# Optimization experiments

Measured on AMD Instinct MI355X. Metric: run time of the kernel, lower is better.

Reference implementation:

```python
import jax, jax.numpy as jnp
import numpy as np

N_NODES = 100_000
N_EDGES = 1_000_000
LATENT = 64
HID_ATOM = 256
HID_BOND = 256
RBF_DIM = 32
RBF_DMAX = 10.0
N_ATOM_TYPES = 10
N_CHARGES = 6
N_BOND_ORDERS = 5


def setup_inputs() -> dict:
    key = jax.random.key(0)
    ks = jax.random.split(key, 12)
    positions = jax.random.normal(ks[0], (N_NODES, 3), dtype=jnp.float32) * 5.0
    quantized = jax.random.normal(ks[1], (N_NODES, LATENT), dtype=jnp.float32)
    pair_indices = jax.random.randint(ks[2], (N_EDGES, 2), 0, N_NODES, dtype=jnp.int64)
    s = 0.05
    return {
        "positions": positions,
        "quantized": quantized,
        "pair_indices": pair_indices,
        "aW1": jax.random.normal(ks[3], (LATENT, HID_ATOM), jnp.float32) * s,
        "ab1": jnp.zeros((HID_ATOM,), jnp.float32),
        "aW2": jax.random.normal(ks[4], (HID_ATOM, N_ATOM_TYPES + N_CHARGES), jnp.float32) * s,
        "ab2": jnp.zeros((N_ATOM_TYPES + N_CHARGES,), jnp.float32),
        "bW1": jax.random.normal(ks[5], (LATENT + RBF_DIM, HID_BOND), jnp.float32) * s,
        "bb1": jnp.zeros((HID_BOND,), jnp.float32),
        "bW2": jax.random.normal(ks[6], (HID_BOND, N_BOND_ORDERS), jnp.float32) * s,
        "bb2": jnp.zeros((N_BOND_ORDERS,), jnp.float32),
    }


def _norm_no_nan(x, eps=1e-8):
    # L2 norm over last axis, clamped to avoid NaN gradients at 0
    return jnp.sqrt(jnp.maximum(jnp.sum(x * x, axis=-1), eps))


def _rbf(D, D_min=0.0, D_max=RBF_DMAX, D_count=RBF_DIM):
    mu = jnp.linspace(D_min, D_max, D_count, dtype=D.dtype)  # [D_count]
    sigma = (D_max - D_min) / D_count
    z = (D[..., None] - mu) / sigma
    return jnp.exp(-z * z)  # [E, D_count]


def reference(positions, quantized, pair_indices, aW1, ab1, aW2, ab2, bW1, bb1, bW2, bb2):
    src = pair_indices[:, 0]
    dst = pair_indices[:, 1]
    # pairwise distances -> RBF expansion
    x_i = positions[src]            # [E, 3]
    x_j = positions[dst]
    dists = _rbf(_norm_no_nan(x_i - x_j))  # [E, rbf_dim]
    # atom decoder (per node)
    h = jax.nn.relu(quantized @ aW1 + ab1)
    scalar_logits = h @ aW2 + ab2
    atom_type_logits = scalar_logits[:, :N_ATOM_TYPES]
    atom_charge_logits = scalar_logits[:, N_ATOM_TYPES:]
    # bond decoder (per edge): gathered latent sum concat RBF
    pair_feats = quantized[src] + quantized[dst]           # [E, latent]
    combined = jnp.concatenate([pair_feats, dists], axis=1)  # [E, latent+rbf]
    hb = jax.nn.relu(combined @ bW1 + bb1)
    bond_order_logits = hb @ bW2 + bb2
    return (atom_type_logits, atom_charge_logits, bond_order_logits)
```

## Files before the change

kernel.cpp:

```cpp
#include <hip/hip_runtime.h>
#include <hip/hip_bf16.h>

typedef __bf16 bf16x8 __attribute__((ext_vector_type(8)));
typedef __bf16 bf16x4 __attribute__((ext_vector_type(4)));
typedef float  f32x4  __attribute__((ext_vector_type(4)));
typedef short  s16x4  __attribute__((ext_vector_type(4)));

#define N_NODES 100000
#define N_EDGES 1000000
#define LATENT  64
#define HID     256
#define RBF_DIM 32
#define NTYPES  10
#define NCHG    6
#define NBOND   5

#define ATOM_TILES (N_NODES / 32)
#define ANBLK 512

#define ETILE  32
#define ETILES (N_EDGES / ETILE)
#define ENBLK  1280

static __device__ __forceinline__ f32x4 mfma16(bf16x4 a, bf16x4 b, f32x4 c) {
#if __has_builtin(__builtin_amdgcn_mfma_f32_16x16x16bf16_1k)
    s16x4 ai = __builtin_bit_cast(s16x4, a);
    s16x4 bi = __builtin_bit_cast(s16x4, b);
    return __builtin_amdgcn_mfma_f32_16x16x16bf16_1k(ai, bi, c, 0, 0, 0);
#else
    asm volatile("s_nop 1\n\t"
                 "v_mfma_f32_16x16x16_bf16 %0, %1, %2, %0\n\t"
                 "s_nop 7\n\ts_nop 7"
                 : "+v"(c) : "v"(a), "v"(b));
    return c;
#endif
}

struct __align__(16) ASmem {
    __bf16 qs[32][72];
    __bf16 hsE[32][264];
    float  red[4][2][4][64];
};

template<bool EMIT_QB>
__global__ __launch_bounds__(256, 2) void atom_kernel(
    const float* __restrict__ q,   const float* __restrict__ aW1,
    const float* __restrict__ ab1, const float* __restrict__ aW2,
    const float* __restrict__ ab2, float* __restrict__ outA,
    float* __restrict__ outB,      __bf16* __restrict__ qb,
    const float* __restrict__ pos, const int* __restrict__ pair,
    float* __restrict__ dist)
{
    __shared__ ASmem sm;
    const int t    = threadIdx.x;
    const int w    = t >> 6;
    const int lane = t & 63;
    const int l15  = lane & 15;
    const int hi   = lane >> 4;
    const int wcol = w * 64;

    bf16x8 aw1f[2][4];
    #pragma unroll
    for (int kb = 0; kb < 2; ++kb)
        #pragma unroll
        for (int nt = 0; nt < 4; ++nt) {
            const int nn = wcol + nt * 16 + l15;
            const int k0 = kb * 32 + hi * 8;
            bf16x8 v;
            #pragma unroll
            for (int j = 0; j < 8; ++j) v[j] = (__bf16)aW1[(k0 + j) * HID + nn];
            aw1f[kb][nt] = v;
        }
    bf16x8 aw2f[2];
    #pragma unroll
    for (int kk = 0; kk < 2; ++kk) {
        const int k0 = (w * 2 + kk) * 32 + hi * 8;
        bf16x8 v;
        #pragma unroll
        for (int j = 0; j < 8; ++j) v[j] = (__bf16)aW2[(k0 + j) * 16 + l15];
        aw2f[kk] = v;
    }
    float4 b1v[4];
    #pragma unroll
    for (int nt = 0; nt < 4; ++nt)
        b1v[nt] = *(const float4*)(&ab1[wcol + nt * 16 + hi * 4]);

    const int m_st = t >> 3;
    const int p_st = t & 7;

    for (int tile = blockIdx.x; tile < ATOM_TILES; tile += ANBLK) {
        const int node0 = tile * 32;
        {
            const float* qr = q + (size_t)(node0 + m_st) * 64 + p_st * 8;
            const float4 a0 = *(const float4*)(qr);
            const float4 a1 = *(const float4*)(qr + 4);
            bf16x8 v;
            v[0] = (__bf16)a0.x; v[1] = (__bf16)a0.y; v[2] = (__bf16)a0.z; v[3] = (__bf16)a0.w;
            v[4] = (__bf16)a1.x; v[5] = (__bf16)a1.y; v[6] = (__bf16)a1.z; v[7] = (__bf16)a1.w;
            *(bf16x8*)(&sm.qs[m_st][p_st * 8]) = v;
            if constexpr (EMIT_QB)
                *(bf16x8*)(qb + (size_t)(node0 + m_st) * 64 + p_st * 8) = v;
        }
        __syncthreads();

        f32x4 acc[2][4];
        #pragma unroll
        for (int mt = 0; mt < 2; ++mt)
            #pragma unroll
            for (int nt = 0; nt < 4; ++nt)
                #pragma unroll
                for (int r = 0; r < 4; ++r)
                    acc[mt][nt][r] = ((const float*)&b1v[nt])[r];

        #pragma unroll
        for (int kb = 0; kb < 2; ++kb)
            #pragma unroll
            for (int mt = 0; mt < 2; ++mt) {
                const bf16x8 bq = *(const bf16x8*)((const char*)&sm.qs[0][0]
                                   + (mt * 16 + l15) * 144 + kb * 64 + hi * 16);
                #pragma unroll
                for (int nt = 0; nt < 4; ++nt)
                    acc[mt][nt] = __builtin_amdgcn_mfma_f32_16x16x32_bf16(
                        aw1f[kb][nt], bq, acc[mt][nt], 0, 0, 0);
            }

        #pragma unroll
        for (int mt = 0; mt < 2; ++mt)
            #pragma unroll
            for (int nt = 0; nt < 4; ++nt) {
                bf16x4 hv;
                #pragma unroll
                for (int r = 0; r < 4; ++r)
                    hv[r] = (__bf16)fmaxf(acc[mt][nt][r], 0.f);
                *(bf16x4*)(&sm.hsE[mt * 16 + l15][wcol + nt * 16 + hi * 4]) = hv;
            }
        __syncthreads();

        f32x4 acc2[2];
        {
            f32x4 z = {0.f, 0.f, 0.f, 0.f};
            acc2[0] = z; acc2[1] = z;
        }
        #pragma unroll
        for (int mt = 0; mt < 2; ++mt)
            #pragma unroll
            for (int kk = 0; kk < 2; ++kk) {
                const int kb = w * 2 + kk;
                const bf16x8 af = *(const bf16x8*)((const char*)&sm.hsE[0][0]
                                   + (mt * 16 + l15) * 528 + kb * 64 + hi * 16);
                acc2[mt] = __builtin_amdgcn_mfma_f32_16x16x32_bf16(
                    af, aw2f[kk], acc2[mt], 0, 0, 0);
            }
        #pragma unroll
        for (int mt = 0; mt < 2; ++mt)
            #pragma unroll
            for (int r = 0; r < 4; ++r)
                sm.red[w][mt][r][lane] = acc2[mt][r];
        __syncthreads();

        {
            const int o  = t & 15;
            const int m0 = t >> 4;
            #pragma unroll
            for (int half = 0; half < 2; ++half) {
                const int m  = m0 + half * 16;
                const int mt = m >> 4, rr = m & 15;
                const int hh = rr >> 2, r = rr & 3;
                float s = ab2[o];
                #pragma unroll
                for (int ww = 0; ww < 4; ++ww) s += sm.red[ww][mt][r][hh * 16 + o];
                const int node = node0 + m;
                if (o < NTYPES) outA[node * NTYPES + o] = s;
                else            outB[node * NCHG + (o - NTYPES)] = s;
            }
        }
        __syncthreads();
    }

    if constexpr (EMIT_QB) {
        for (int e = blockIdx.x * 256 + t; e < N_EDGES; e += ANBLK * 256) {
            const int2 pr = ((const int2*)pair)[e];
            const float dx = pos[(unsigned)pr.x * 3u]      - pos[(unsigned)pr.y * 3u];
            const float dy = pos[(unsigned)pr.x * 3u + 1u] - pos[(unsigned)pr.y * 3u + 1u];
            const float dz = pos[(unsigned)pr.x * 3u + 2u] - pos[(unsigned)pr.y * 3u + 2u];
            dist[e] = sqrtf(fmaxf(dx * dx + dy * dy + dz * dz, 1e-8f));
        }
    }
}

struct __align__(16) ESmem {
    __bf16 comb[2][ETILE][104];
    float  red[2][4][2][4][64];
};

__device__ __forceinline__ void bar_lgkm() {
    asm volatile("s_waitcnt lgkmcnt(0)" ::: "memory");
    __builtin_amdgcn_s_barrier();
}

template<bool USEBF>
__global__ __launch_bounds__(256, 3) void edge_kernel(
    const float* __restrict__ pos, const float* __restrict__ qf,
    const __bf16* __restrict__ qb, const float* __restrict__ dist,
    const int* __restrict__ pair,
    const float* __restrict__ bW1, const float* __restrict__ bb1,
    const float* __restrict__ bW2, const float* __restrict__ bb2,
    float* __restrict__ outC)
{
    __shared__ ESmem sm;
    const int t    = threadIdx.x;
    const int w    = t >> 6;
    const int lane = t & 63;
    const int l15  = lane & 15;
    const int hi   = lane >> 4;
    const int hid0 = w * 64;

    bf16x8 bw1f[3][4];
    #pragma unroll
    for (int kb = 0; kb < 3; ++kb)
        #pragma unroll
        for (int nt = 0; nt < 4; ++nt) {
            const int nn = hid0 + nt * 16 + l15;
            const int k0 = kb * 32 + hi * 8;
            bf16x8 v;
            #pragma unroll
            for (int j = 0; j < 8; ++j) v[j] = (__bf16)bW1[(k0 + j) * HID + nn];
            bw1f[kb][nt] = v;
        }
    bf16x4 w2f[4];
    #pragma unroll
    for (int nt = 0; nt < 4; ++nt) {
        bf16x4 v;
        #pragma unroll
        for (int j = 0; j < 4; ++j)
            v[j] = (l15 < NBOND)
                 ? (__bf16)bW2[(hid0 + nt * 16 + hi * 4 + j) * NBOND + l15]
                 : (__bf16)0.f;
        w2f[nt] = v;
    }
    float4 b1v[4];
    #pragma unroll
    for (int nt = 0; nt < 4; ++nt)
        b1v[nt] = *(const float4*)(&bb1[hid0 + nt * 16 + hi * 4]);

    const int e_loc = t >> 3;
    const int p     = t & 7;

    int tile = blockIdx.x;
    bf16x8 gs, gd;
    float  Dv;
    float4 fs0, fs1, fd0, fd1;
    float  ps0, ps1, ps2, pd0, pd1, pd2;

    #define GATHER(pN, tg)                                                        \
        if constexpr (USEBF) {                                                    \
            gs = *(const bf16x8*)(qb + ((unsigned)(pN).x * 64u + (unsigned)(p*8)));\
            gd = *(const bf16x8*)(qb + ((unsigned)(pN).y * 64u + (unsigned)(p*8)));\
            Dv = dist[(size_t)(tg) * ETILE + e_loc];                              \
        } else {                                                                  \
            fs0 = *(const float4*)(qf + ((unsigned)(pN).x * 64u + (unsigned)(p*8)));     \
            fs1 = *(const float4*)(qf + ((unsigned)(pN).x * 64u + (unsigned)(p*8) + 4u));\
            fd0 = *(const float4*)(qf + ((unsigned)(pN).y * 64u + (unsigned)(p*8)));     \
            fd1 = *(const float4*)(qf + ((unsigned)(pN).y * 64u + (unsigned)(p*8) + 4u));\
            ps0 = pos[(unsigned)(pN).x * 3u];  ps1 = pos[(unsigned)(pN).x * 3u + 1u];    \
            ps2 = pos[(unsigned)(pN).x * 3u + 2u];                                \
            pd0 = pos[(unsigned)(pN).y * 3u];  pd1 = pos[(unsigned)(pN).y * 3u + 1u];    \
            pd2 = pos[(unsigned)(pN).y * 3u + 2u];                                \
        }

    #define STAGE(buf)                                                            \
        {                                                                         \
            bf16x8 cv;                                                            \
            float D;                                                              \
            if constexpr (USEBF) {                                                \
                _Pragma("unroll")                                                 \
                for (int j = 0; j < 8; ++j)                                       \
                    cv[j] = (__bf16)((float)gs[j] + (float)gd[j]);                \
                D = Dv;                                                           \
            } else {                                                              \
                cv[0] = (__bf16)(fs0.x + fd0.x); cv[1] = (__bf16)(fs0.y + fd0.y); \
                cv[2] = (__bf16)(fs0.z + fd0.z); cv[3] = (__bf16)(fs0.w + fd0.w); \
                cv[4] = (__bf16)(fs1.x + fd1.x); cv[5] = (__bf16)(fs1.y + fd1.y); \
                cv[6] = (__bf16)(fs1.z + fd1.z); cv[7] = (__bf16)(fs1.w + fd1.w); \
                const float dx = ps0 - pd0, dy = ps1 - pd1, dz = ps2 - pd2;       \
                D = sqrtf(fmaxf(dx * dx + dy * dy + dz * dz, 1e-8f));             \
            }                                                                     \
            *(bf16x8*)(&sm.comb[buf][e_loc][p * 8]) = cv;                         \
            bf16x4 rv;                                                            \
            _Pragma("unroll")                                                     \
            for (int j = 0; j < 4; ++j) {                                         \
                const float mu = (float)(p * 4 + j) * (10.0f / 31.0f);            \
                const float z  = (D - mu) * 3.2f;                                 \
                rv[j] = (__bf16)__expf(-z * z);                                   \
            }                                                                     \
            *(bf16x4*)(&sm.comb[buf][e_loc][64 + p * 4]) = rv;                    \
        }

    int  tgA = tile;
    int2 pA  = ((const int2*)pair)[(size_t)tile * ETILE + e_loc];
    GATHER(pA, tgA);
    tgA = (tile + ENBLK < ETILES) ? tile + ENBLK : 0;
    pA  = ((const int2*)pair)[(size_t)tgA * ETILE + e_loc];
    STAGE(0);
    GATHER(pA, tgA);
    tgA = (tile + 2 * ENBLK < ETILES) ? tile + 2 * ENBLK : 0;
    pA  = ((const int2*)pair)[(size_t)tgA * ETILE + e_loc];
    bar_lgkm();

    int cur = 0;
    int e0_prev = -1;

    for (; tile < ETILES; tile += ENBLK) {
        const int e0 = tile * ETILE;

        if (e0_prev >= 0 && t < 160) {
            const int m = t / 5, o = t % 5;
            const int mt = m >> 4, rr = m & 15;
            const int hh = rr >> 2, r = rr & 3;
            float s = bb2[o];
            #pragma unroll
            for (int ww = 0; ww < 4; ++ww)
                s += sm.red[cur ^ 1][ww][mt][r][hh * 16 + o];
            outC[(size_t)(e0_prev + m) * NBOND + o] = s;
        }

        STAGE(cur ^ 1);

        GATHER(pA, tgA);
        tgA = (tile + 3 * ENBLK < ETILES) ? tile + 3 * ENBLK : 0;
        pA  = ((const int2*)pair)[(size_t)tgA * ETILE + e_loc];

        f32x4 acc[2][4];
        #pragma unroll
        for (int mt = 0; mt < 2; ++mt)
            #pragma unroll
            for (int nt = 0; nt < 4; ++nt)
                #pragma unroll
                for (int r = 0; r < 4; ++r)
                    acc[mt][nt][r] = ((const float*)&b1v[nt])[r];

        #pragma unroll
        for (int kb = 0; kb < 3; ++kb)
            #pragma unroll
            for (int mt = 0; mt < 2; ++mt) {
                const bf16x8 bf = *(const bf16x8*)((const char*)&sm.comb[cur][0][0]
                                   + (mt * 16 + l15) * 208 + kb * 64 + hi * 16);
                #pragma unroll
                for (int nt = 0; nt < 4; ++nt)
                    acc[mt][nt] = __builtin_amdgcn_mfma_f32_16x16x32_bf16(
                        bw1f[kb][nt], bf, acc[mt][nt], 0, 0, 0);
            }

        {
            f32x4 acc2[2];
            {
                f32x4 z = {0.f, 0.f, 0.f, 0.f};
                acc2[0] = z; acc2[1] = z;
            }
            #pragma unroll
            for (int mt = 0; mt < 2; ++mt)
                #pragma unroll
                for (int nt = 0; nt < 4; ++nt) {
                    bf16x4 hv;
                    #pragma unroll
                    for (int r = 0; r < 4; ++r)
                        hv[r] = (__bf16)fmaxf(acc[mt][nt][r], 0.f);
                    acc2[mt] = mfma16(hv, w2f[nt], acc2[mt]);
                }
            #pragma unroll
            for (int mt = 0; mt < 2; ++mt)
                #pragma unroll
                for (int r = 0; r < 4; ++r)
                    sm.red[cur][w][mt][r][lane] = acc2[mt][r];
        }

        e0_prev = e0;
        bar_lgkm();
        cur ^= 1;
    }

    if (e0_prev >= 0 && t < 160) {
        const int m = t / 5, o = t % 5;
        const int mt = m >> 4, rr = m & 15;
        const int hh = rr >> 2, r = rr & 3;
        float s = bb2[o];
        #pragma unroll
        for (int ww = 0; ww < 4; ++ww)
            s += sm.red[cur ^ 1][ww][mt][r][hh * 16 + o];
        outC[(size_t)(e0_prev + m) * NBOND + o] = s;
    }
    #undef GATHER
    #undef STAGE
}

extern "C" void kernel_launch(void* const* d_in, const int* in_sizes, int n_in,
                              void* d_out, int out_size, void* d_ws, size_t ws_size,
                              hipStream_t stream)
{
    const float* pos = (const float*)d_in[0];
    const float* q   = (const float*)d_in[1];
    const int*   pair= (const int*)  d_in[2];
    const float* aW1 = (const float*)d_in[3];
    const float* ab1 = (const float*)d_in[4];
    const float* aW2 = (const float*)d_in[5];
    const float* ab2 = (const float*)d_in[6];
    const float* bW1 = (const float*)d_in[7];
    const float* bb1 = (const float*)d_in[8];
    const float* bW2 = (const float*)d_in[9];
    const float* bb2 = (const float*)d_in[10];

    float* out  = (float*)d_out;
    float* outA = out;
    float* outB = out + (size_t)N_NODES * NTYPES;
    float* outC = out + (size_t)N_NODES * (NTYPES + NCHG);

    const size_t qb_bytes   = (size_t)N_NODES * LATENT * sizeof(__bf16);
    const size_t dist_bytes = (size_t)N_EDGES * sizeof(float);
    const bool use_bf = (ws_size >= qb_bytes + dist_bytes);
    __bf16* qb   = (__bf16*)d_ws;
    float*  dist = (float*)((char*)d_ws + qb_bytes);

    if (use_bf)
        hipLaunchKernelGGL(atom_kernel<true>, dim3(ANBLK), dim3(256), 0, stream,
                           q, aW1, ab1, aW2, ab2, outA, outB, qb, pos, pair, dist);
    else
        hipLaunchKernelGGL(atom_kernel<false>, dim3(ANBLK), dim3(256), 0, stream,
                           q, aW1, ab1, aW2, ab2, outA, outB, qb, pos, pair, dist);

    if (use_bf)
        hipLaunchKernelGGL(edge_kernel<true>, dim3(ENBLK), dim3(256), 0, stream,
                           pos, q, qb, dist, pair, bW1, bb1, bW2, bb2, outC);
    else
        hipLaunchKernelGGL(edge_kernel<false>, dim3(ENBLK), dim3(256), 0, stream,
                           pos, q, qb, dist, pair, bW1, bb1, bW2, bb2, outC);
}
```

Measured before the change: 113.3 us.

## Split distance kernel, store src/dst latents separately, and shrink edge grid

```diff
diff --git a/kernel.cpp b/kernel.cpp
--- a/kernel.cpp
+++ b/kernel.cpp
@@ -20,7 +20,7 @@
 
 #define ETILE  32
 #define ETILES (N_EDGES / ETILE)
-#define ENBLK  1280
+#define ENBLK  768
 
 static __device__ __forceinline__ f32x4 mfma16(bf16x4 a, bf16x4 b, f32x4 c) {
 #if __has_builtin(__builtin_amdgcn_mfma_f32_16x16x16bf16_1k)
@@ -36,6 +36,19 @@
 #endif
 }
 
+__global__ __launch_bounds__(256) void dist_kernel(
+    const float* __restrict__ pos, const int* __restrict__ pair,
+    float* __restrict__ dist)
+{
+    const int e = blockIdx.x * 256 + threadIdx.x;
+    if (e >= N_EDGES) return;
+    const int2 pr = ((const int2*)pair)[e];
+    const float dx = pos[(unsigned)pr.x * 3u]      - pos[(unsigned)pr.y * 3u];
+    const float dy = pos[(unsigned)pr.x * 3u + 1u] - pos[(unsigned)pr.y * 3u + 1u];
+    const float dz = pos[(unsigned)pr.x * 3u + 2u] - pos[(unsigned)pr.y * 3u + 2u];
+    dist[e] = sqrtf(fmaxf(dx * dx + dy * dy + dz * dz, 1e-8f));
+}
+
 struct __align__(16) ASmem {
     __bf16 qs[32][72];
     __bf16 hsE[32][264];
@@ -47,9 +60,7 @@
     const float* __restrict__ q,   const float* __restrict__ aW1,
     const float* __restrict__ ab1, const float* __restrict__ aW2,
     const float* __restrict__ ab2, float* __restrict__ outA,
-    float* __restrict__ outB,      __bf16* __restrict__ qb,
-    const float* __restrict__ pos, const int* __restrict__ pair,
-    float* __restrict__ dist)
+    float* __restrict__ outB,      __bf16* __restrict__ qb)
 {
     __shared__ ASmem sm;
     const int t    = threadIdx.x;
@@ -176,20 +187,10 @@
         }
         __syncthreads();
     }
-
-    if constexpr (EMIT_QB) {
-        for (int e = blockIdx.x * 256 + t; e < N_EDGES; e += ANBLK * 256) {
-            const int2 pr = ((const int2*)pair)[e];
-            const float dx = pos[(unsigned)pr.x * 3u]      - pos[(unsigned)pr.y * 3u];
-            const float dy = pos[(unsigned)pr.x * 3u + 1u] - pos[(unsigned)pr.y * 3u + 1u];
-            const float dz = pos[(unsigned)pr.x * 3u + 2u] - pos[(unsigned)pr.y * 3u + 2u];
-            dist[e] = sqrtf(fmaxf(dx * dx + dy * dy + dz * dz, 1e-8f));
-        }
-    }
 }
 
 struct __align__(16) ESmem {
-    __bf16 comb[2][ETILE][104];
+    __bf16 comb[2][ETILE][168];
     float  red[2][4][2][4][64];
 };
 
@@ -246,6 +247,10 @@
     const int e_loc = t >> 3;
     const int p     = t & 7;
 
+    const int ep_m  = t / 5, ep_o = t % 5;
+    const int ep_mt = ep_m >> 4;
+    const int ep_hh = (ep_m & 15) >> 2, ep_r = ep_m & 3;
+
     int tile = blockIdx.x;
     bf16x8 gs, gd;
     float  Dv;
@@ -270,22 +275,27 @@
 
     #define STAGE(buf)                                                            \
         {                                                                         \
-            bf16x8 cv;                                                            \
+            char* rowp = (char*)&sm.comb[buf][0][0] + e_loc * 336;                \
             float D;                                                              \
             if constexpr (USEBF) {                                                \
-                _Pragma("unroll")                                                 \
-                for (int j = 0; j < 8; ++j)                                       \
-                    cv[j] = (__bf16)((float)gs[j] + (float)gd[j]);                \
+                *(bf16x8*)(rowp + p * 16)       = gs;                             \
+                *(bf16x8*)(rowp + 128 + p * 16) = gd;                             \
                 D = Dv;                                                           \
             } else {                                                              \
-                cv[0] = (__bf16)(fs0.x + fd0.x); cv[1] = (__bf16)(fs0.y + fd0.y); \
-                cv[2] = (__bf16)(fs0.z + fd0.z); cv[3] = (__bf16)(fs0.w + fd0.w); \
-                cv[4] = (__bf16)(fs1.x + fd1.x); cv[5] = (__bf16)(fs1.y + fd1.y); \
-                cv[6] = (__bf16)(fs1.z + fd1.z); cv[7] = (__bf16)(fs1.w + fd1.w); \
+                bf16x8 vs, vd;                                                    \
+                vs[0] = (__bf16)fs0.x; vs[1] = (__bf16)fs0.y;                     \
+                vs[2] = (__bf16)fs0.z; vs[3] = (__bf16)fs0.w;                     \
+                vs[4] = (__bf16)fs1.x; vs[5] = (__bf16)fs1.y;                     \
+                vs[6] = (__bf16)fs1.z; vs[7] = (__bf16)fs1.w;                     \
+                vd[0] = (__bf16)fd0.x; vd[1] = (__bf16)fd0.y;                     \
+                vd[2] = (__bf16)fd0.z; vd[3] = (__bf16)fd0.w;                     \
+                vd[4] = (__bf16)fd1.x; vd[5] = (__bf16)fd1.y;                     \
+                vd[6] = (__bf16)fd1.z; vd[7] = (__bf16)fd1.w;                     \
+                *(bf16x8*)(rowp + p * 16)       = vs;                             \
+                *(bf16x8*)(rowp + 128 + p * 16) = vd;                             \
                 const float dx = ps0 - pd0, dy = ps1 - pd1, dz = ps2 - pd2;       \
                 D = sqrtf(fmaxf(dx * dx + dy * dy + dz * dz, 1e-8f));             \
             }                                                                     \
-            *(bf16x8*)(&sm.comb[buf][e_loc][p * 8]) = cv;                         \
             bf16x4 rv;                                                            \
             _Pragma("unroll")                                                     \
             for (int j = 0; j < 4; ++j) {                                         \
@@ -293,7 +303,7 @@
                 const float z  = (D - mu) * 3.2f;                                 \
                 rv[j] = (__bf16)__expf(-z * z);                                   \
             }                                                                     \
-            *(bf16x4*)(&sm.comb[buf][e_loc][64 + p * 4]) = rv;                    \
+            *(bf16x4*)(rowp + 256 + p * 8) = rv;                                  \
         }
 
     int  tgA = tile;
@@ -314,14 +324,11 @@
         const int e0 = tile * ETILE;
 
         if (e0_prev >= 0 && t < 160) {
-            const int m = t / 5, o = t % 5;
-            const int mt = m >> 4, rr = m & 15;
-            const int hh = rr >> 2, r = rr & 3;
-            float s = bb2[o];
+            float s = bb2[ep_o];
             #pragma unroll
             for (int ww = 0; ww < 4; ++ww)
-                s += sm.red[cur ^ 1][ww][mt][r][hh * 16 + o];
-            outC[(size_t)(e0_prev + m) * NBOND + o] = s;
+                s += sm.red[cur ^ 1][ww][ep_mt][ep_r][ep_hh * 16 + ep_o];
+            outC[(size_t)(e0_prev + ep_m) * NBOND + ep_o] = s;
         }
 
         STAGE(cur ^ 1);
@@ -340,16 +347,18 @@
                     acc[mt][nt][r] = ((const float*)&b1v[nt])[r];
 
         #pragma unroll
-        for (int kb = 0; kb < 3; ++kb)
+        for (int kb = 0; kb < 5; ++kb) {
+            const int kbu = (kb < 2) ? kb : ((kb < 4) ? kb - 2 : 2);
             #pragma unroll
             for (int mt = 0; mt < 2; ++mt) {
                 const bf16x8 bf = *(const bf16x8*)((const char*)&sm.comb[cur][0][0]
-                                   + (mt * 16 + l15) * 208 + kb * 64 + hi * 16);
+                                   + (mt * 16 + l15) * 336 + kb * 64 + hi * 16);
                 #pragma unroll
                 for (int nt = 0; nt < 4; ++nt)
                     acc[mt][nt] = __builtin_amdgcn_mfma_f32_16x16x32_bf16(
-                        bw1f[kb][nt], bf, acc[mt][nt], 0, 0, 0);
-            }
+                        bw1f[kbu][nt], bf, acc[mt][nt], 0, 0, 0);
+            }
+        }
 
         {
             f32x4 acc2[2];
@@ -380,14 +389,11 @@
     }
 
     if (e0_prev >= 0 && t < 160) {
-        const int m = t / 5, o = t % 5;
-        const int mt = m >> 4, rr = m & 15;
-        const int hh = rr >> 2, r = rr & 3;
-        float s = bb2[o];
+        float s = bb2[ep_o];
         #pragma unroll
         for (int ww = 0; ww < 4; ++ww)
-            s += sm.red[cur ^ 1][ww][mt][r][hh * 16 + o];
-        outC[(size_t)(e0_prev + m) * NBOND + o] = s;
+            s += sm.red[cur ^ 1][ww][ep_mt][ep_r][ep_hh * 16 + ep_o];
+        outC[(size_t)(e0_prev + ep_m) * NBOND + ep_o] = s;
     }
     #undef GATHER
     #undef STAGE
@@ -420,17 +426,17 @@
     __bf16* qb   = (__bf16*)d_ws;
     float*  dist = (float*)((char*)d_ws + qb_bytes);
 
-    if (use_bf)
+    if (use_bf) {
+        hipLaunchKernelGGL(dist_kernel, dim3((N_EDGES + 255) / 256), dim3(256),
+                           0, stream, pos, pair, dist);
         hipLaunchKernelGGL(atom_kernel<true>, dim3(ANBLK), dim3(256), 0, stream,
-                           q, aW1, ab1, aW2, ab2, outA, outB, qb, pos, pair, dist);
-    else
-        hipLaunchKernelGGL(atom_kernel<false>, dim3(ANBLK), dim3(256), 0, stream,
-                           q, aW1, ab1, aW2, ab2, outA, outB, qb, pos, pair, dist);
-
-    if (use_bf)
+                           q, aW1, ab1, aW2, ab2, outA, outB, qb);
         hipLaunchKernelGGL(edge_kernel<true>, dim3(ENBLK), dim3(256), 0, stream,
                            pos, q, qb, dist, pair, bW1, bb1, bW2, bb2, outC);
-    else
+    } else {
+        hipLaunchKernelGGL(atom_kernel<false>, dim3(ANBLK), dim3(256), 0, stream,
+                           q, aW1, ab1, aW2, ab2, outA, outB, qb);
         hipLaunchKernelGGL(edge_kernel<false>, dim3(ENBLK), dim3(256), 0, stream,
                            pos, q, qb, dist, pair, bW1, bb1, bW2, bb2, outC);
-}
+    }
+}
```

Result: slower. 121.4 us (+7.1%).
